# Optimization experiments

Measured on AMD Instinct MI355X. Metric: run time of the kernel, lower is better.

## Reference

```python
import jax, jax.numpy as jnp
import numpy as np

CURRENT_TIME = 1000.0
TIME_WEIGHT = 0.1
NEG_INF = -1e9


def setup_inputs() -> dict:
    key = jax.random.key(0)
    ks = jax.random.split(key, 7)
    B, M, D, C = 1024, 65536, 64, 16
    return {
        "query": jax.random.normal(ks[0], (B, D), dtype=jnp.float32),
        "context": jax.random.normal(ks[1], (B, C), dtype=jnp.float32),
        "mem_keys": jax.random.normal(ks[2], (M, D), dtype=jnp.float32) * 0.1,
        "mem_values": jax.random.normal(ks[3], (M, D), dtype=jnp.float32) * 0.1,
        "mem_contexts": jax.random.normal(ks[4], (M, C), dtype=jnp.float32) * 0.1,
        "mem_timestamps": jax.random.uniform(ks[5], (M, 1), dtype=jnp.float32) * CURRENT_TIME,
        "used_mask": jax.random.randint(ks[6], (M,), 0, 2) > 0,
    }


def reference(query, context, mem_keys, mem_values, mem_contexts, mem_timestamps, used_mask):
    # content score: [B, M]
    scores = jnp.einsum("bd,md->bm", query, mem_keys)
    # context score, scaled by 0.5
    scores = scores + 0.5 * jnp.einsum("bc,mc->bm", context, mem_contexts)
    # time-decay bias, scaled by 0.3 (broadcast over batch)
    decay = jnp.exp(-TIME_WEIGHT * (CURRENT_TIME - mem_timestamps[:, 0]))  # [M]
    scores = scores + 0.3 * decay[None, :]
    # unused slots get -1e9 exactly as torch.full init
    scores = jnp.where(used_mask[None, :], scores, NEG_INF)
    attn = jax.nn.softmax(scores, axis=-1)
    return jnp.einsum("bm,md->bd", attn, mem_values)
```

## Files before the change

### kernel.cpp

```cpp
#include <hip/hip_runtime.h>

typedef float f32x4 __attribute__((ext_vector_type(4)));
typedef __bf16 bf16x8 __attribute__((ext_vector_type(8)));
typedef unsigned int u32;
typedef unsigned short u16;

#define MTOT 65536
#define BTOT 1024
#define DD 64
#define LOG2E 1.44269504088896340736f
#define MFMA __builtin_amdgcn_mfma_f32_16x16x32_bf16

#define NROWBLK ((MTOT + BTOT) * 24 / 256)
#define NVTBLK  (MTOT / 64)
#define ESPACE  (DD * BTOT + BTOT)
#define NSLICE  8

__device__ __forceinline__ u16 f2bf(float f) { return __builtin_bit_cast(u16, (__bf16)f); }
__device__ __forceinline__ u32 pk2(float a, float b) {
    return (u32)f2bf(a) | ((u32)f2bf(b) << 16);
}
__device__ __forceinline__ bf16x8 ldg8(const u16* p) { return *reinterpret_cast<const bf16x8*>(p); }
__device__ __forceinline__ float fexp2(float x) {
#if __has_builtin(__builtin_amdgcn_exp2f)
    return __builtin_amdgcn_exp2f(x);
#else
    return exp2f(x);
#endif
}
__device__ __forceinline__ void glds16(const void* g, void* l) {
    __builtin_amdgcn_global_load_lds((const __attribute__((address_space(1))) u32*)g,
                                     (__attribute__((address_space(3))) u32*)l, 16, 0, 0);
}

__global__ __launch_bounds__(256)
void k_count(const int* __restrict__ mask, int* __restrict__ blockCount)
{
    int t = threadIdx.x;
    int m = blockIdx.x * 256 + t;
    int active = mask[m] != 0;
    unsigned long long bal = __ballot(active);
    __shared__ int wc[4];
    if ((t & 63) == 0) wc[t >> 6] = __popcll(bal);
    __syncthreads();
    if (t == 0) blockCount[blockIdx.x] = wc[0] + wc[1] + wc[2] + wc[3];
}

__global__ __launch_bounds__(256)
void k_scan(const int* __restrict__ blockCount, int* __restrict__ blockOff,
            int* __restrict__ MaPtr)
{
    __shared__ int sdata[256];
    int t = threadIdx.x;
    int v = blockCount[t];
    sdata[t] = v;
    __syncthreads();
#pragma unroll
    for (int off = 1; off < 256; off <<= 1) {
        int x = (t >= off) ? sdata[t - off] : 0;
        __syncthreads();
        sdata[t] += x;
        __syncthreads();
    }
    blockOff[t] = sdata[t] - v;
    if (t == 255) *MaPtr = sdata[255];
}

__global__ __launch_bounds__(256)
void k_scatter(const int* __restrict__ mask, const float* __restrict__ TS,
               const int* __restrict__ blockOff,
               int* __restrict__ idxc, float* __restrict__ biasc)
{
    int t = threadIdx.x;
    int m = blockIdx.x * 256 + t;
    int active = mask[m] != 0;
    unsigned long long bal = __ballot(active);
    int lane = t & 63, wid = t >> 6;
    __shared__ int wc[4];
    if (lane == 0) wc[wid] = __popcll(bal);
    __syncthreads();
    int base = blockOff[blockIdx.x];
    for (int w = 0; w < wid; ++w) base += wc[w];
    int rank = __popcll(bal & ((1ull << lane) - 1ull));
    if (active) {
        int dst = base + rank;
        idxc[dst]  = m;
        biasc[dst] = 0.3f * __expf(-0.1f * (1000.0f - TS[m]));
    }
}

__global__ __launch_bounds__(256)
void prep_all(const float* __restrict__ q, const float* __restrict__ ctx,
              const float* __restrict__ K, const float* __restrict__ CT,
              const float* __restrict__ V,
              const int* __restrict__ MaPtr, const int* __restrict__ idxc,
              const float* __restrict__ biasc,
              u16* __restrict__ Qc, u16* __restrict__ KC, u16* __restrict__ Vt)
{
    __shared__ u16 L[64][68];
    const int blk = blockIdx.x, t = threadIdx.x;
    const int Ma = *MaPtr;

    if (blk < NROWBLK) {
        const int R = MTOT + BTOT;
        int gid = blk * 256 + t;
        float4 v = {0.f, 0.f, 0.f, 0.f};
        u16* dst;
        if (gid < R * 16) {
            int row = gid >> 4, qd = gid & 15;
            bool isQ = row >= MTOT;
            if (isQ) {
                int r2 = row - MTOT;
                v = *reinterpret_cast<const float4*>(q + (size_t)r2 * 64 + qd * 4);
                v.x *= LOG2E; v.y *= LOG2E; v.z *= LOG2E; v.w *= LOG2E;
                dst = Qc + (size_t)r2 * 96 + qd * 4;
            } else {
                if (row < Ma)
                    v = *reinterpret_cast<const float4*>(K + (size_t)idxc[row] * 64 + qd * 4);
                dst = KC + (size_t)row * 96 + qd * 4;
            }
        } else if (gid < R * 20) {
            int i = gid - R * 16;
            int row = i >> 2, qd = i & 3;
            bool isQ = row >= MTOT;
            if (isQ) {
                int r2 = row - MTOT;
                v = *reinterpret_cast<const float4*>(ctx + (size_t)r2 * 16 + qd * 4);
                const float s = 0.5f * LOG2E; v.x *= s; v.y *= s; v.z *= s; v.w *= s;
                dst = Qc + (size_t)r2 * 96 + 64 + qd * 4;
            } else {
                if (row < Ma)
                    v = *reinterpret_cast<const float4*>(CT + (size_t)idxc[row] * 16 + qd * 4);
                dst = KC + (size_t)row * 96 + 64 + qd * 4;
            }
        } else {
            int i = gid - R * 20;
            int row = i >> 2, qd = i & 3;
            bool isQ = row >= MTOT;
            if (isQ) {
                int r2 = row - MTOT;
                if (qd == 0) v.x = LOG2E;
                dst = Qc + (size_t)r2 * 96 + 80 + qd * 4;
            } else {
                if (qd == 0) v.x = (row < Ma) ? biasc[row] : -1000.0f;
                dst = KC + (size_t)row * 96 + 80 + qd * 4;
            }
        }
        ushort4 o = { f2bf(v.x), f2bf(v.y), f2bf(v.z), f2bf(v.w) };
        *reinterpret_cast<ushort4*>(dst) = o;
        return;
    }

    const int m0 = (blk - NROWBLK) * 64;
#pragma unroll
    for (int p = 0; p < 4; ++p) {
        int fi = t + p * 256;
        int mi = fi >> 4, di = (fi & 15) << 2;
        int r = m0 + mi;
        float4 v = {0.f, 0.f, 0.f, 0.f};
        if (r < Ma)
            v = *reinterpret_cast<const float4*>(V + (size_t)idxc[r] * 64 + di);
        ushort4 o = { f2bf(v.x), f2bf(v.y), f2bf(v.z), f2bf(v.w) };
        *reinterpret_cast<ushort4*>(&L[mi][di]) = o;
    }
    __syncthreads();
    const int d = t >> 2, seg = t & 3;
    u32 pk[8];
#pragma unroll
    for (int pr = 0; pr < 8; ++pr) {
        int c0 = seg * 16 + pr * 2;
        int g32 = c0 >> 5;
        int i0 = c0 & 31, i1 = (c0 + 1) & 31;
        int mp0 = g32 * 32 + (i0 >> 1) + (i0 & 1) * 16;
        int mp1 = g32 * 32 + (i1 >> 1) + (i1 & 1) * 16;
        pk[pr] = (u32)L[mp0][d] | ((u32)L[mp1][d] << 16);
    }
    uint4 A = {pk[0], pk[1], pk[2], pk[3]}, B4 = {pk[4], pk[5], pk[6], pk[7]};
    u16* dst = Vt + (size_t)d * MTOT + m0 + seg * 16;
    *reinterpret_cast<uint4*>(dst)     = A;
    *reinterpret_cast<uint4*>(dst + 8) = B4;
}

__global__ __launch_bounds__(512, 4)
void epmem_mfma(const u16* __restrict__ Qc, const u16* __restrict__ KCg,
                const u16* __restrict__ Vtg, const int* __restrict__ MaPtr,
                float* __restrict__ pl, float* __restrict__ pacc,
                int SPLIT, int NB)
{
    __shared__ __align__(16) u16 KCs[2][64 * 96];
    __shared__ __align__(16) u16 Vts[2][64 * 64];
    __shared__ __align__(16) u16 Pb[8][32][40];

    const int tid = threadIdx.x;
    const int w = tid >> 6, lane = tid & 63;
    const int l15 = lane & 15, g = lane >> 4;

    const int bid = blockIdx.x;
    const int o = (bid & 7) * (NB >> 3) + (bid >> 3);
    const int rt = o & 3, ch = o >> 2;
    const int rbase = rt * 256 + w * 32;

    const u16* qp = Qc + (size_t)(rbase + l15) * 96 + g * 8;
    bf16x8 qf[2][3];
#pragma unroll
    for (int sb = 0; sb < 2; ++sb)
#pragma unroll
        for (int c = 0; c < 3; ++c)
            qf[sb][c] = ldg8(qp + sb * 16 * 96 + c * 32);

    const int Ma = *MaPtr;
    const int Mpad = (Ma + 63) & ~63;
    const int mper = ((Mpad + SPLIT - 1) / SPLIT + 63) & ~63;
    const int m0 = ch * mper;
    const int m1 = (m0 + mper < Mpad) ? (m0 + mper) : Mpad;
    const int ntiles = (m1 > m0) ? ((m1 - m0) >> 6) : 0;

    int kgo[3], vgo[2];
    if (w < 4) {
#pragma unroll
        for (int i = 0; i < 3; ++i) {
            int ol = w * 3072 + i * 1024 + lane * 16;
            int row = ol / 192;
            int c = (ol - row * 192) >> 4;
            int u = (c < 8) ? (c ^ (row & 7)) : (8 + ((c & 3) ^ (row & 3)));
            kgo[i] = row * 192 + u * 16;
        }
#pragma unroll
        for (int i = 0; i < 2; ++i) {
            int ol = w * 2048 + i * 1024 + lane * 16;
            int row = ol >> 7, c = (ol >> 4) & 7;
            int u = c ^ (row & 7);
            vgo[i] = row * (MTOT * 2) + u * 16;
        }
    }

    const u32 ow = (l15 == 0) ? 0x3F803F80u : 0u;
    const uint4 ou = {ow, ow, ow, ow};
    const bf16x8 onesf = __builtin_bit_cast(bf16x8, ou);

    f32x4 acc[2][4];
    f32x4 accl[2];
#pragma unroll
    for (int sb = 0; sb < 2; ++sb) {
        accl[sb] = (f32x4){0, 0, 0, 0};
#pragma unroll
        for (int d4 = 0; d4 < 4; ++d4) acc[sb][d4] = (f32x4){0, 0, 0, 0};
    }

    if (ntiles > 0 && w < 4) {
        const char* kb = (const char*)KCg + (size_t)m0 * 192;
        const char* vb = (const char*)Vtg + (size_t)m0 * 2;
#pragma unroll
        for (int i = 0; i < 3; ++i) glds16(kb + kgo[i], (char*)KCs[0] + w * 3072 + i * 1024);
#pragma unroll
        for (int i = 0; i < 2; ++i) glds16(vb + vgo[i], (char*)Vts[0] + w * 2048 + i * 1024);
    }
    __syncthreads();

    char* pbw = (char*)Pb[w];
    const int xr = l15 & 7;
    const int x3 = l15 & 3;

    int cur = 0;
    for (int t = 0; t < ntiles; ++t) {
        if (t + 1 < ntiles && w < 4) {
            int mt = m0 + ((t + 1) << 6);
            const char* kb = (const char*)KCg + (size_t)mt * 192;
            const char* vb = (const char*)Vtg + (size_t)mt * 2;
            int nb = cur ^ 1;
#pragma unroll
            for (int i = 0; i < 3; ++i) glds16(kb + kgo[i], (char*)KCs[nb] + w * 3072 + i * 1024);
#pragma unroll
            for (int i = 0; i < 2; ++i) glds16(vb + vgo[i], (char*)Vts[nb] + w * 2048 + i * 1024);
        }
        const char* kcb = (const char*)KCs[cur];
        const char* vtb = (const char*)Vts[cur];

#pragma unroll
        for (int j = 0; j < 2; ++j) {
            bf16x8 kf[2][3];
#pragma unroll
            for (int s = 0; s < 2; ++s) {
                int row = j * 32 + s * 16 + l15;
                kf[s][0] = *reinterpret_cast<const bf16x8*>(kcb + row * 192 + (((0 + g) ^ xr) << 4));
                kf[s][1] = *reinterpret_cast<const bf16x8*>(kcb + row * 192 + (((4 + g) ^ xr) << 4));
                kf[s][2] = *reinterpret_cast<const bf16x8*>(kcb + row * 192 + ((8 + (g ^ x3)) << 4));
            }
            bf16x8 vf[4];
#pragma unroll
            for (int d4 = 0; d4 < 4; ++d4) {
                int row = d4 * 16 + l15;
                vf[d4] = *reinterpret_cast<const bf16x8*>(vtb + row * 128 + (((j * 4 + g) ^ xr) << 4));
            }

            f32x4 S00 = {0,0,0,0}, S01 = {0,0,0,0}, S10 = {0,0,0,0}, S11 = {0,0,0,0};
            S00 = MFMA(qf[0][0], kf[0][0], S00,0,0,0); S00 = MFMA(qf[0][1], kf[0][1], S00,0,0,0); S00 = MFMA(qf[0][2], kf[0][2], S00,0,0,0);
            S01 = MFMA(qf[0][0], kf[1][0], S01,0,0,0); S01 = MFMA(qf[0][1], kf[1][1], S01,0,0,0); S01 = MFMA(qf[0][2], kf[1][2], S01,0,0,0);
            S10 = MFMA(qf[1][0], kf[0][0], S10,0,0,0); S10 = MFMA(qf[1][1], kf[0][1], S10,0,0,0); S10 = MFMA(qf[1][2], kf[0][2], S10,0,0,0);
            S11 = MFMA(qf[1][0], kf[1][0], S11,0,0,0); S11 = MFMA(qf[1][1], kf[1][1], S11,0,0,0); S11 = MFMA(qf[1][2], kf[1][2], S11,0,0,0);

#pragma unroll
            for (int r = 0; r < 4; ++r) {
                float p00 = fexp2(S00[r]), p01 = fexp2(S01[r]);
                float p10 = fexp2(S10[r]), p11 = fexp2(S11[r]);
                int row0 = g * 4 + r, row1 = 16 + g * 4 + r;
                int cw = (((l15 >> 2) ^ r) << 4) | ((l15 & 3) << 2);
                *(u32*)(pbw + row0 * 80 + cw) = pk2(p00, p01);
                *(u32*)(pbw + row1 * 80 + cw) = pk2(p10, p11);
            }
            bf16x8 pa0 = *reinterpret_cast<const bf16x8*>(pbw + l15 * 80        + ((g ^ x3) << 4));
            bf16x8 pa1 = *reinterpret_cast<const bf16x8*>(pbw + (16 + l15) * 80 + ((g ^ x3) << 4));

            acc[0][0] = MFMA(pa0, vf[0], acc[0][0],0,0,0); acc[0][1] = MFMA(pa0, vf[1], acc[0][1],0,0,0);
            acc[0][2] = MFMA(pa0, vf[2], acc[0][2],0,0,0); acc[0][3] = MFMA(pa0, vf[3], acc[0][3],0,0,0);
            acc[1][0] = MFMA(pa1, vf[0], acc[1][0],0,0,0); acc[1][1] = MFMA(pa1, vf[1], acc[1][1],0,0,0);
            acc[1][2] = MFMA(pa1, vf[2], acc[1][2],0,0,0); acc[1][3] = MFMA(pa1, vf[3], acc[1][3],0,0,0);
            accl[0] = MFMA(pa0, onesf, accl[0],0,0,0);
            accl[1] = MFMA(pa1, onesf, accl[1],0,0,0);
        }
        __syncthreads();
        cur ^= 1;
    }

    if (l15 == 0) {
#pragma unroll
        for (int sb = 0; sb < 2; ++sb)
            *reinterpret_cast<f32x4*>(pl + (size_t)ch * BTOT + rbase + sb * 16 + g * 4) = accl[sb];
    }

    float* bp = pacc + ((size_t)ch * DD + l15) * BTOT + rbase + g * 4;
#pragma unroll
    for (int sb = 0; sb < 2; ++sb)
#pragma unroll
        for (int d4 = 0; d4 < 4; ++d4)
            *reinterpret_cast<f32x4*>(bp + (size_t)(d4 * 16) * BTOT + sb * 16) = acc[sb][d4];
}

__global__ __launch_bounds__(256)
void combineA(const float* __restrict__ pl, const float* __restrict__ pacc,
              float* __restrict__ part, int cper)
{
    int e = blockIdx.x * 256 + threadIdx.x;
    int s = blockIdx.y;
    int c0 = s * cper;
    float v0 = 0.f, v1 = 0.f;
    if (e < DD * BTOT) {
        const float* p = pacc + (size_t)c0 * (DD * BTOT) + e;
#pragma unroll 2
        for (int i = 0; i + 1 < cper; i += 2) {
            v0 += p[(size_t)i * (DD * BTOT)];
            v1 += p[(size_t)(i + 1) * (DD * BTOT)];
        }
        if (cper & 1) v0 += p[(size_t)(cper - 1) * (DD * BTOT)];
    } else {
        const float* p = pl + (size_t)c0 * BTOT + (e - DD * BTOT);
#pragma unroll 2
        for (int i = 0; i + 1 < cper; i += 2) {
            v0 += p[(size_t)i * BTOT];
            v1 += p[(size_t)(i + 1) * BTOT];
        }
        if (cper & 1) v0 += p[(size_t)(cper - 1) * BTOT];
    }
    part[(size_t)s * ESPACE + e] = v0 + v1;
}

__global__ __launch_bounds__(256)
void combineB(const float* __restrict__ part, float* __restrict__ out)
{
    int t = blockIdx.x * 256 + threadIdx.x;
    int d = t >> 10, b = t & 1023;
    float v = 0.f, lssum = 0.f;
#pragma unroll
    for (int s = 0; s < NSLICE; ++s) {
        v     += part[(size_t)s * ESPACE + t];
        lssum += part[(size_t)s * ESPACE + DD * BTOT + b];
    }
    out[(size_t)b * DD + d] = v / lssum;
}

extern "C" void kernel_launch(void* const* d_in, const int* in_sizes, int n_in,
                              void* d_out, int out_size, void* d_ws, size_t ws_size,
                              hipStream_t stream)
{
    const float* q    = (const float*)d_in[0];
    const float* ctx  = (const float*)d_in[1];
    const float* K    = (const float*)d_in[2];
    const float* V    = (const float*)d_in[3];
    const float* CT   = (const float*)d_in[4];
    const float* TS   = (const float*)d_in[5];
    const int*   mask = (const int*)d_in[6];

    char* wsb = (char*)d_ws;
    u16* Qc = (u16*)(wsb);
    u16* KC = (u16*)(wsb + 196608);
    u16* Vt = (u16*)(wsb + 196608 + 12582912);
    size_t fixed = 196608 + 12582912 + 8388608;

    int*   MaPtr      = (int*)(wsb + fixed);
    int*   blockCount = (int*)(wsb + fixed + 4096);
    int*   blockOff   = (int*)(wsb + fixed + 8192);
    int*   idxc       = (int*)(wsb + fixed + 12288);
    float* biasc      = (float*)(wsb + fixed + 12288 + 262144);
    size_t scratch_end = fixed + 12288 + 524288;

    size_t chunk = (size_t)BTOT * (DD + 1) * sizeof(float);
    size_t partB = (size_t)NSLICE * ESPACE * sizeof(float);
    int SPLIT = (int)((ws_size - scratch_end - partB) / chunk);
    if (SPLIT > 128) SPLIT = 128;
    SPLIT &= ~7;
    if (SPLIT < 8) SPLIT = 8;

    float* pl   = (float*)(wsb + scratch_end);
    float* pacc = pl + (size_t)SPLIT * BTOT;
    float* part = pacc + (size_t)SPLIT * DD * BTOT;

    int cper = SPLIT / NSLICE;

    k_count  <<<MTOT / 256, 256, 0, stream>>>(mask, blockCount);
    k_scan   <<<1, 256, 0, stream>>>(blockCount, blockOff, MaPtr);
    k_scatter<<<MTOT / 256, 256, 0, stream>>>(mask, TS, blockOff, idxc, biasc);

    prep_all<<<NROWBLK + NVTBLK, 256, 0, stream>>>(q, ctx, K, CT, V, MaPtr, idxc, biasc,
                                                   Qc, KC, Vt);

    int NB = 4 * SPLIT;
    epmem_mfma<<<NB, 512, 0, stream>>>(Qc, KC, Vt, MaPtr, pl, pacc, SPLIT, NB);

    dim3 gA((ESPACE + 255) / 256, NSLICE);
    combineA<<<gA, 256, 0, stream>>>(pl, pacc, part, cper);
    combineB<<<(DD * BTOT) / 256, 256, 0, stream>>>(part, (float*)d_out);
}
```

Before: 56.91 us.

## Store split-K partial accumulators as bf16 and skip prep work past active rows

The attention kernel now writes its per-chunk partial output accumulators as packed bf16 instead of fp32, and combineA reads pairs of bf16 values and widens them to fp32 for the reduction. This halves the partial-accumulator traffic between the main kernel and the combine pass. The prep kernel also returns early for key/context rows beyond the active count and for V-transpose blocks beyond the padded active count, so it no longer writes zeros there. The bf16 partials lose precision in the cross-chunk sum, and the skipped rows in KC/Vt are left unwritten, relying on the main kernel never reading past the padded count.

```diff
diff --git a/kernel.cpp b/kernel.cpp
--- a/kernel.cpp
+++ b/kernel.cpp
@@ -100,6 +100,7 @@
     __shared__ u16 L[64][68];
     const int blk = blockIdx.x, t = threadIdx.x;
     const int Ma = *MaPtr;
+    const int Mpad = (Ma + 63) & ~63;
 
     if (blk < NROWBLK) {
         const int R = MTOT + BTOT;
@@ -115,8 +116,8 @@
                 v.x *= LOG2E; v.y *= LOG2E; v.z *= LOG2E; v.w *= LOG2E;
                 dst = Qc + (size_t)r2 * 96 + qd * 4;
             } else {
-                if (row < Ma)
-                    v = *reinterpret_cast<const float4*>(K + (size_t)idxc[row] * 64 + qd * 4);
+                if (row >= Ma) return;
+                v = *reinterpret_cast<const float4*>(K + (size_t)idxc[row] * 64 + qd * 4);
                 dst = KC + (size_t)row * 96 + qd * 4;
             }
         } else if (gid < R * 20) {
@@ -129,8 +130,8 @@
                 const float s = 0.5f * LOG2E; v.x *= s; v.y *= s; v.z *= s; v.w *= s;
                 dst = Qc + (size_t)r2 * 96 + 64 + qd * 4;
             } else {
-                if (row < Ma)
-                    v = *reinterpret_cast<const float4*>(CT + (size_t)idxc[row] * 16 + qd * 4);
+                if (row >= Ma) return;
+                v = *reinterpret_cast<const float4*>(CT + (size_t)idxc[row] * 16 + qd * 4);
                 dst = KC + (size_t)row * 96 + 64 + qd * 4;
             }
         } else {
@@ -142,6 +143,7 @@
                 if (qd == 0) v.x = LOG2E;
                 dst = Qc + (size_t)r2 * 96 + 80 + qd * 4;
             } else {
+                if (row >= Mpad) return;
                 if (qd == 0) v.x = (row < Ma) ? biasc[row] : -1000.0f;
                 dst = KC + (size_t)row * 96 + 80 + qd * 4;
             }
@@ -152,6 +154,7 @@
     }
 
     const int m0 = (blk - NROWBLK) * 64;
+    if (m0 >= Mpad) return;
 #pragma unroll
     for (int p = 0; p < 4; ++p) {
         int fi = t + p * 256;
@@ -184,7 +187,7 @@
 __global__ __launch_bounds__(512, 4)
 void epmem_mfma(const u16* __restrict__ Qc, const u16* __restrict__ KCg,
                 const u16* __restrict__ Vtg, const int* __restrict__ MaPtr,
-                float* __restrict__ pl, float* __restrict__ pacc,
+                float* __restrict__ pl, u16* __restrict__ paccb,
                 int SPLIT, int NB)
 {
     __shared__ __align__(16) u16 KCs[2][64 * 96];
@@ -328,40 +331,42 @@
             *reinterpret_cast<f32x4*>(pl + (size_t)ch * BTOT + rbase + sb * 16 + g * 4) = accl[sb];
     }
 
-    float* bp = pacc + ((size_t)ch * DD + l15) * BTOT + rbase + g * 4;
 #pragma unroll
     for (int sb = 0; sb < 2; ++sb)
 #pragma unroll
-        for (int d4 = 0; d4 < 4; ++d4)
-            *reinterpret_cast<f32x4*>(bp + (size_t)(d4 * 16) * BTOT + sb * 16) = acc[sb][d4];
-}
-
-__global__ __launch_bounds__(256)
-void combineA(const float* __restrict__ pl, const float* __restrict__ pacc,
+        for (int d4 = 0; d4 < 4; ++d4) {
+            uint2 wv;
+            wv.x = pk2(acc[sb][d4][0], acc[sb][d4][1]);
+            wv.y = pk2(acc[sb][d4][2], acc[sb][d4][3]);
+            *reinterpret_cast<uint2*>(paccb + ((size_t)ch * DD + d4 * 16 + l15) * BTOT
+                                      + rbase + sb * 16 + g * 4) = wv;
+        }
+}
+
+__global__ __launch_bounds__(256)
+void combineA(const float* __restrict__ pl, const u32* __restrict__ paccb,
               float* __restrict__ part, int cper)
 {
-    int e = blockIdx.x * 256 + threadIdx.x;
+    int e2 = blockIdx.x * 256 + threadIdx.x;
     int s = blockIdx.y;
     int c0 = s * cper;
-    float v0 = 0.f, v1 = 0.f;
-    if (e < DD * BTOT) {
-        const float* p = pacc + (size_t)c0 * (DD * BTOT) + e;
-#pragma unroll 2
-        for (int i = 0; i + 1 < cper; i += 2) {
-            v0 += p[(size_t)i * (DD * BTOT)];
-            v1 += p[(size_t)(i + 1) * (DD * BTOT)];
-        }
-        if (cper & 1) v0 += p[(size_t)(cper - 1) * (DD * BTOT)];
+    if (e2 < (DD * BTOT / 2)) {
+        const u32* p = paccb + (size_t)c0 * (DD * BTOT / 2) + e2;
+        float s0 = 0.f, s1 = 0.f;
+        for (int i = 0; i < cper; ++i) {
+            u32 v = p[(size_t)i * (DD * BTOT / 2)];
+            s0 += __uint_as_float(v << 16);
+            s1 += __uint_as_float(v & 0xFFFF0000u);
+        }
+        float2 o = {s0, s1};
+        *reinterpret_cast<float2*>(part + (size_t)s * ESPACE + 2 * e2) = o;
     } else {
-        const float* p = pl + (size_t)c0 * BTOT + (e - DD * BTOT);
-#pragma unroll 2
-        for (int i = 0; i + 1 < cper; i += 2) {
-            v0 += p[(size_t)i * BTOT];
-            v1 += p[(size_t)(i + 1) * BTOT];
-        }
-        if (cper & 1) v0 += p[(size_t)(cper - 1) * BTOT];
-    }
-    part[(size_t)s * ESPACE + e] = v0 + v1;
+        int b = e2 - DD * BTOT / 2;
+        const float* p = pl + (size_t)c0 * BTOT + b;
+        float v0 = 0.f;
+        for (int i = 0; i < cper; ++i) v0 += p[(size_t)i * BTOT];
+        part[(size_t)s * ESPACE + DD * BTOT + b] = v0;
+    }
 }
 
 __global__ __launch_bounds__(256)
@@ -403,16 +408,16 @@
     float* biasc      = (float*)(wsb + fixed + 12288 + 262144);
     size_t scratch_end = fixed + 12288 + 524288;
 
-    size_t chunk = (size_t)BTOT * (DD + 1) * sizeof(float);
+    size_t chunk = (size_t)BTOT * 4 + (size_t)DD * BTOT * 2;
     size_t partB = (size_t)NSLICE * ESPACE * sizeof(float);
     int SPLIT = (int)((ws_size - scratch_end - partB) / chunk);
     if (SPLIT > 128) SPLIT = 128;
     SPLIT &= ~7;
     if (SPLIT < 8) SPLIT = 8;
 
-    float* pl   = (float*)(wsb + scratch_end);
-    float* pacc = pl + (size_t)SPLIT * BTOT;
-    float* part = pacc + (size_t)SPLIT * DD * BTOT;
+    float* pl    = (float*)(wsb + scratch_end);
+    u16*   paccb = (u16*)(pl + (size_t)SPLIT * BTOT);
+    float* part  = (float*)(paccb + (size_t)SPLIT * DD * BTOT);
 
     int cper = SPLIT / NSLICE;
 
@@ -424,9 +429,9 @@
                                                    Qc, KC, Vt);
 
     int NB = 4 * SPLIT;
-    epmem_mfma<<<NB, 512, 0, stream>>>(Qc, KC, Vt, MaPtr, pl, pacc, SPLIT, NB);
-
-    dim3 gA((ESPACE + 255) / 256, NSLICE);
-    combineA<<<gA, 256, 0, stream>>>(pl, pacc, part, cper);
+    epmem_mfma<<<NB, 512, 0, stream>>>(Qc, KC, Vt, MaPtr, pl, paccb, SPLIT, NB);
+
+    dim3 gA((DD * BTOT / 2 + BTOT + 255) / 256, NSLICE);
+    combineA<<<gA, 256, 0, stream>>>(pl, (const u32*)paccb, part, cper);
     combineB<<<(DD * BTOT) / 256, 256, 0, stream>>>(part, (float*)d_out);
 }
```

New measurement: 54.43 us. -4.4%, faster.
